# Kernel optimization log

Measured on AMD Instinct MI355X. Metric: run time of the kernel, lower is better.

## Reference

```python
import jax, jax.numpy as jnp
import numpy as np

WH, WW = 7, 7
NUM_HEADS = 16
DIM = 512
NW = 64  # windows per image (56/7)^2


def _relative_position_index(wh, ww):
    coords = np.stack(np.meshgrid(np.arange(wh), np.arange(ww), indexing='ij'))  # 2,wh,ww
    cf = coords.reshape(2, -1)
    rel = cf[:, :, None] - cf[:, None, :]            # 2,N,N
    rel = rel.transpose(1, 2, 0).astype(np.int32)    # N,N,2
    rel[:, :, 0] += wh - 1
    rel[:, :, 1] += ww - 1
    rel[:, :, 0] *= 2 * ww - 1
    return jnp.asarray(rel.sum(-1))                  # N,N int32


def setup_inputs() -> dict:
    key = jax.random.key(0)
    ks = jax.random.split(key, 7)
    B_, N, C = 2048, WH * WW, DIM
    x = jax.random.normal(ks[0], (B_, N, C), dtype=jnp.float32)
    # 0 / -100 shifted-window mask pattern
    mask = jnp.where(jax.random.uniform(ks[1], (NW, N, N)) < 0.8, 0.0, -100.0).astype(jnp.float32)
    qkv_w = jax.random.normal(ks[2], (3 * C, C), dtype=jnp.float32) * 0.02
    qkv_b = jax.random.normal(ks[3], (3 * C,), dtype=jnp.float32) * 0.02
    proj_w = jax.random.normal(ks[4], (C, C), dtype=jnp.float32) * 0.02
    proj_b = jax.random.normal(ks[5], (C,), dtype=jnp.float32) * 0.02
    rel_bias_table = jax.random.normal(ks[6], ((2 * WH - 1) * (2 * WW - 1), NUM_HEADS), dtype=jnp.float32) * 0.02
    rel_index = _relative_position_index(WH, WW)
    return {"x": x, "mask": mask, "qkv_w": qkv_w, "qkv_b": qkv_b,
            "proj_w": proj_w, "proj_b": proj_b,
            "rel_bias_table": rel_bias_table, "rel_index": rel_index}


def reference(x, mask, qkv_w, qkv_b, proj_w, proj_b, rel_bias_table, rel_index):
    B_, N, C = x.shape
    H = NUM_HEADS
    hd = C // H
    scale = hd ** -0.5
    qkv = x @ qkv_w.T + qkv_b                         # B_,N,3C
    qkv = qkv.reshape(B_, N, 3, H, hd).transpose(2, 0, 3, 1, 4)  # 3,B_,H,N,hd
    q, k, v = qkv[0] * scale, qkv[1], qkv[2]
    attn = jnp.einsum('bhnd,bhmd->bhnm', q, k)        # B_,H,N,N
    # gathered relative position bias -> H,N,N
    bias = rel_bias_table[rel_index.reshape(-1)].reshape(N, N, H).transpose(2, 0, 1)
    attn = attn + bias[None]
    nW = mask.shape[0]
    attn = attn.reshape(B_ // nW, nW, H, N, N) + mask[None, :, None]
    attn = jax.nn.softmax(attn.reshape(B_, H, N, N), axis=-1)
    out = jnp.einsum('bhnm,bhmd->bhnd', attn, v).transpose(0, 2, 1, 3).reshape(B_, N, C)
    return out @ proj_w.T + proj_b
```

## Files before the change

kernel.cpp:

```cpp
#include <hip/hip_runtime.h>

typedef unsigned short u16;
typedef short s16x8 __attribute__((ext_vector_type(8)));
typedef __bf16 bf16x8 __attribute__((ext_vector_type(8)));
typedef float f32x4 __attribute__((ext_vector_type(4)));


__device__ __forceinline__ u16 f2bf(float f) {
  union { float f; unsigned u; } x; x.f = f;
  unsigned r = (x.u + 0x7fffu + ((x.u >> 16) & 1u)) >> 16;
  return (u16)r;
}

__device__ __forceinline__ f32x4 mfma_bf16_16x16x32(s16x8 a, s16x8 b, f32x4 c) {
  return __builtin_amdgcn_mfma_f32_16x16x32_bf16(
      __builtin_bit_cast(bf16x8, a), __builtin_bit_cast(bf16x8, b), c, 0, 0, 0);
}

__device__ __forceinline__ void gl_lds16(const u16* g, u16* l) {
  __builtin_amdgcn_global_load_lds(
      (__attribute__((address_space(1))) unsigned int*)g,
      (__attribute__((address_space(3))) unsigned int*)l, 16, 0, 0);
}


__global__ __launch_bounds__(256) void cvt_bf16(const float* __restrict__ src,
                                                u16* __restrict__ dst, int n) {
  int i = (blockIdx.x * 256 + threadIdx.x) * 4;
  if (i + 3 < n) {
    float4 f = *(const float4*)(src + i);
    ushort4 o;
    o.x = f2bf(f.x); o.y = f2bf(f.y); o.z = f2bf(f.z); o.w = f2bf(f.w);
    *(ushort4*)(dst + i) = o;
  }
}

__global__ __launch_bounds__(256) void build_bias(const float* __restrict__ tbl,
                                                  const int* __restrict__ ridx,
                                                  float* __restrict__ biasf) {
  int t = blockIdx.x * 256 + threadIdx.x;
  if (t < 16 * 2401) {
    int h = t / 2401, ij = t % 2401;
    biasf[t] = tbl[ridx[ij] * 16 + h];
  }
}


template <bool OUT_BF16>
__global__ __launch_bounds__(256) void gemm_bt(const u16* __restrict__ A,
                                               const u16* __restrict__ B,
                                               const float* __restrict__ bias,
                                               void* __restrict__ C,
                                               int M, int N, int K) {
  __shared__ u16 As[128 * 32];
  __shared__ u16 Bs[128 * 32];
  const int t = threadIdx.x;
  const int w = t >> 6, l = t & 63;
  const int quad = l >> 4, lo = l & 15;
  const long m0 = (long)blockIdx.y * 128;
  const long n0 = (long)blockIdx.x * 128;
  const int wm = (w >> 1) * 64, wn = (w & 1) * 64;

  f32x4 acc[4][4] = {};

  const int srow0 = w * 32 + (l >> 2);
  const int skc = (l & 3) * 8;
  const u16* gA = A + (m0 + srow0) * (long)K + skc;
  const u16* gB = B + (n0 + srow0) * (long)K + skc;
  u16* lA = As + (w * 128 + l) * 8;
  u16* lB = Bs + (w * 128 + l) * 8;

  for (int k0 = 0; k0 < K; k0 += 32) {
    gl_lds16(gA + k0, lA);
    gl_lds16(gA + 16 * (long)K + k0, lA + 64 * 8);
    gl_lds16(gB + k0, lB);
    gl_lds16(gB + 16 * (long)K + k0, lB + 64 * 8);
    __syncthreads();

    s16x8 af[4], bfv[4];
#pragma unroll
    for (int i = 0; i < 4; ++i) {
      af[i]  = *(const s16x8*)(As + (wm + i * 16 + lo) * 32 + quad * 8);
      bfv[i] = *(const s16x8*)(Bs + (wn + i * 16 + lo) * 32 + quad * 8);
    }
#pragma unroll
    for (int mt = 0; mt < 4; ++mt)
#pragma unroll
      for (int nt = 0; nt < 4; ++nt)
        acc[mt][nt] = mfma_bf16_16x16x32(af[mt], bfv[nt], acc[mt][nt]);
    __syncthreads();
  }

#pragma unroll
  for (int mt = 0; mt < 4; ++mt) {
#pragma unroll
    for (int nt = 0; nt < 4; ++nt) {
      long col = n0 + wn + nt * 16 + lo;
      float bv = bias[col];
      long rowb = m0 + wm + mt * 16 + quad * 4;
#pragma unroll
      for (int r = 0; r < 4; ++r) {
        float v = acc[mt][nt][r] + bv;
        long off = (rowb + r) * (long)N + col;
        if (OUT_BF16) ((u16*)C)[off] = f2bf(v);
        else          ((float*)C)[off] = v;
      }
    }
  }
}


__global__ __launch_bounds__(256) void attn_kernel(const u16* __restrict__ qkv,
                                                   const float* __restrict__ biasf,
                                                   const float* __restrict__ mask,
                                                   u16* __restrict__ ao) {
  __shared__ u16 P[4][64 * 64];
  const int t = threadIdx.x;
  const int w = t >> 6, l = t & 63;
  const int quad = l >> 4, lo = l & 15;
  const int u = blockIdx.x * 4 + w;
  const int b = u >> 4, h = u & 15;

  const u16* qp = qkv + (long)b * 49 * 1536 + h * 32;
  const u16* kp = qp + 512;
  const u16* vp = qp + 1024;

  const s16x8 zero8 = {};
  s16x8 qf[4], kf[4];
#pragma unroll
  for (int mt = 0; mt < 4; ++mt) {
    int m = mt * 16 + lo;
    qf[mt] = (m < 49) ? *(const s16x8*)(qp + (long)m * 1536 + quad * 8) : zero8;
    kf[mt] = (m < 49) ? *(const s16x8*)(kp + (long)m * 1536 + quad * 8) : zero8;
  }

  f32x4 S[4][4] = {};
#pragma unroll
  for (int mt = 0; mt < 4; ++mt)
#pragma unroll
    for (int nt = 0; nt < 4; ++nt)
      S[mt][nt] = mfma_bf16_16x16x32(qf[mt], kf[nt], S[mt][nt]);

  const float scale = 0.17677669529663687f;
  const float* bh = biasf + h * 2401;
  const float* mw = mask + (long)(b & 63) * 2401;

#pragma unroll
  for (int mt = 0; mt < 4; ++mt) {
#pragma unroll
    for (int r = 0; r < 4; ++r) {
      int row = mt * 16 + quad * 4 + r;
      int rr = row < 49 ? row : 48;
      float vals[4];
#pragma unroll
      for (int nt = 0; nt < 4; ++nt) {
        int col = nt * 16 + lo;
        vals[nt] = (col < 49)
                       ? S[mt][nt][r] * scale + bh[rr * 49 + col] + mw[rr * 49 + col]
                       : -1e30f;
      }
      float rm = fmaxf(fmaxf(vals[0], vals[1]), fmaxf(vals[2], vals[3]));
#pragma unroll
      for (int off = 1; off < 16; off <<= 1) rm = fmaxf(rm, __shfl_xor(rm, off, 16));
      float s = 0.f;
#pragma unroll
      for (int nt = 0; nt < 4; ++nt) {
        vals[nt] = __expf(vals[nt] - rm);
        s += vals[nt];
      }
#pragma unroll
      for (int off = 1; off < 16; off <<= 1) s += __shfl_xor(s, off, 16);
      float is = 1.f / s;
#pragma unroll
      for (int nt = 0; nt < 4; ++nt) S[mt][nt][r] = vals[nt] * is;
    }
  }

  u16* pw = &P[w][0];
#pragma unroll
  for (int mt = 0; mt < 4; ++mt)
#pragma unroll
    for (int nt = 0; nt < 4; ++nt)
#pragma unroll
      for (int r = 0; r < 4; ++r)
        pw[(mt * 16 + quad * 4 + r) * 64 + nt * 16 + lo] = f2bf(S[mt][nt][r]);

  f32x4 O[4][2] = {};
#pragma unroll
  for (int kt = 0; kt < 2; ++kt) {
    s16x8 vb[2];
#pragma unroll
    for (int nt = 0; nt < 2; ++nt) {
      union { u16 us[8]; s16x8 v; } tb;
#pragma unroll
      for (int jj = 0; jj < 8; ++jj) {
        int j = kt * 32 + quad * 8 + jj;
        tb.us[jj] = (j < 49) ? vp[(long)j * 1536 + nt * 16 + lo] : (u16)0;
      }
      vb[nt] = tb.v;
    }
#pragma unroll
    for (int mt = 0; mt < 4; ++mt) {
      s16x8 pa = *(const s16x8*)(pw + (mt * 16 + lo) * 64 + kt * 32 + quad * 8);
      O[mt][0] = mfma_bf16_16x16x32(pa, vb[0], O[mt][0]);
      O[mt][1] = mfma_bf16_16x16x32(pa, vb[1], O[mt][1]);
    }
  }

  u16* op = ao + (long)b * 49 * 512 + h * 32;
#pragma unroll
  for (int mt = 0; mt < 4; ++mt)
#pragma unroll
    for (int nt = 0; nt < 2; ++nt)
#pragma unroll
      for (int r = 0; r < 4; ++r) {
        int row = mt * 16 + quad * 4 + r;
        if (row < 49) op[(long)row * 512 + nt * 16 + lo] = f2bf(O[mt][nt][r]);
      }
}


extern "C" void kernel_launch(void* const* d_in, const int* in_sizes, int n_in,
                              void* d_out, int out_size, void* d_ws, size_t ws_size,
                              hipStream_t stream) {
  const float* x      = (const float*)d_in[0];
  const float* mask   = (const float*)d_in[1];
  const float* qkv_w  = (const float*)d_in[2];
  const float* qkv_b  = (const float*)d_in[3];
  const float* proj_w = (const float*)d_in[4];
  const float* proj_b = (const float*)d_in[5];
  const float* tbl    = (const float*)d_in[6];
  const int*   ridx   = (const int*)d_in[7];

  u16* xb    = (u16*)d_ws;
  u16* qkvb  = xb + 51380224;
  u16* wq    = qkvb + 154140672;
  u16* wp    = wq + 786432;
  float* biasf = (float*)(wp + 262144);

  cvt_bf16<<<50176, 256, 0, stream>>>(x, xb, 51380224);
  cvt_bf16<<<768, 256, 0, stream>>>(qkv_w, wq, 786432);
  cvt_bf16<<<256, 256, 0, stream>>>(proj_w, wp, 262144);
  build_bias<<<151, 256, 0, stream>>>(tbl, ridx, biasf);

  gemm_bt<true><<<dim3(12, 784), 256, 0, stream>>>(xb, wq, qkv_b, qkvb,
                                                   100352, 1536, 512);
  attn_kernel<<<8192, 256, 0, stream>>>(qkvb, biasf, mask, xb);

  gemm_bt<false><<<dim3(4, 784), 256, 0, stream>>>(xb, wp, proj_b, d_out,
                                                   100352, 512, 512);
}
```

Baseline: 933.8 us.

## Swizzle LDS layouts, remap GEMM block order, and vectorize epilogue stores

XOR-swizzles the LDS tiles in the GEMM and the P tile in attention to cut bank conflicts on the fragment reads. It remaps the GEMM workgroup order for better L2 locality. It also swaps the MFMA operand order so each lane holds four consecutive output columns, which lets the GEMM and attention epilogues write 8- or 16-byte vectors instead of scattered scalar stores. This adds some index arithmetic, and the changed output layout must stay consistent across the GEMMs and the attention kernel.

```diff
diff --git a/kernel.cpp b/kernel.cpp
--- a/kernel.cpp
+++ b/kernel.cpp
@@ -21,6 +21,10 @@
   __builtin_amdgcn_global_load_lds(
       (__attribute__((address_space(1))) unsigned int*)g,
       (__attribute__((address_space(3))) unsigned int*)l, 16, 0, 0);
+}
+
+__device__ __forceinline__ int p_idx(int row, int col) {
+  return row * 64 + ((((col >> 3) ^ (row & 7)) << 3) | (col & 7));
 }
 
 
@@ -57,14 +61,25 @@
   const int t = threadIdx.x;
   const int w = t >> 6, l = t & 63;
   const int quad = l >> 4, lo = l & 15;
-  const long m0 = (long)blockIdx.y * 128;
-  const long n0 = (long)blockIdx.x * 128;
+
+  int bx = blockIdx.x, by = blockIdx.y;
+  {
+    const int nwg = gridDim.x * gridDim.y;
+    if ((nwg & 7) == 0) {
+      const int lin = bx + gridDim.x * by;
+      const int swz = (lin & 7) * (nwg >> 3) + (lin >> 3);
+      bx = swz % gridDim.x;
+      by = swz / gridDim.x;
+    }
+  }
+  const long m0 = (long)by * 128;
+  const long n0 = (long)bx * 128;
   const int wm = (w >> 1) * 64, wn = (w & 1) * 64;
 
   f32x4 acc[4][4] = {};
 
   const int srow0 = w * 32 + (l >> 2);
-  const int skc = (l & 3) * 8;
+  const int skc = ((l & 3) ^ ((srow0 >> 1) & 3)) * 8;
   const u16* gA = A + (m0 + srow0) * (long)K + skc;
   const u16* gB = B + (n0 + srow0) * (long)K + skc;
   u16* lA = As + (w * 128 + l) * 8;
@@ -80,30 +95,39 @@
     s16x8 af[4], bfv[4];
 #pragma unroll
     for (int i = 0; i < 4; ++i) {
-      af[i]  = *(const s16x8*)(As + (wm + i * 16 + lo) * 32 + quad * 8);
-      bfv[i] = *(const s16x8*)(Bs + (wn + i * 16 + lo) * 32 + quad * 8);
+      const int ra = wm + i * 16 + lo;
+      const int rb = wn + i * 16 + lo;
+      af[i]  = *(const s16x8*)(As + ra * 32 + ((quad ^ ((ra >> 1) & 3)) << 3));
+      bfv[i] = *(const s16x8*)(Bs + rb * 32 + ((quad ^ ((rb >> 1) & 3)) << 3));
     }
 #pragma unroll
     for (int mt = 0; mt < 4; ++mt)
 #pragma unroll
       for (int nt = 0; nt < 4; ++nt)
-        acc[mt][nt] = mfma_bf16_16x16x32(af[mt], bfv[nt], acc[mt][nt]);
+        acc[mt][nt] = mfma_bf16_16x16x32(bfv[nt], af[mt], acc[mt][nt]);
     __syncthreads();
   }
 
 #pragma unroll
   for (int mt = 0; mt < 4; ++mt) {
+    const long m = m0 + wm + mt * 16 + lo;
 #pragma unroll
     for (int nt = 0; nt < 4; ++nt) {
-      long col = n0 + wn + nt * 16 + lo;
-      float bv = bias[col];
-      long rowb = m0 + wm + mt * 16 + quad * 4;
-#pragma unroll
-      for (int r = 0; r < 4; ++r) {
-        float v = acc[mt][nt][r] + bv;
-        long off = (rowb + r) * (long)N + col;
-        if (OUT_BF16) ((u16*)C)[off] = f2bf(v);
-        else          ((float*)C)[off] = v;
+      const long n = n0 + wn + nt * 16 + quad * 4;
+      const float4 bv = *(const float4*)(bias + n);
+      const float v0 = acc[mt][nt][0] + bv.x;
+      const float v1 = acc[mt][nt][1] + bv.y;
+      const float v2 = acc[mt][nt][2] + bv.z;
+      const float v3 = acc[mt][nt][3] + bv.w;
+      const long off = m * (long)N + n;
+      if (OUT_BF16) {
+        uint2 o;
+        o.x = (unsigned)f2bf(v0) | ((unsigned)f2bf(v1) << 16);
+        o.y = (unsigned)f2bf(v2) | ((unsigned)f2bf(v3) << 16);
+        *(uint2*)((u16*)C + off) = o;
+      } else {
+        float4 o = make_float4(v0, v1, v2, v3);
+        *(float4*)((float*)C + off) = o;
       }
     }
   }
@@ -183,7 +207,7 @@
     for (int nt = 0; nt < 4; ++nt)
 #pragma unroll
       for (int r = 0; r < 4; ++r)
-        pw[(mt * 16 + quad * 4 + r) * 64 + nt * 16 + lo] = f2bf(S[mt][nt][r]);
+        pw[p_idx(mt * 16 + quad * 4 + r, nt * 16 + lo)] = f2bf(S[mt][nt][r]);
 
   f32x4 O[4][2] = {};
 #pragma unroll
@@ -201,22 +225,27 @@
     }
 #pragma unroll
     for (int mt = 0; mt < 4; ++mt) {
-      s16x8 pa = *(const s16x8*)(pw + (mt * 16 + lo) * 64 + kt * 32 + quad * 8);
-      O[mt][0] = mfma_bf16_16x16x32(pa, vb[0], O[mt][0]);
-      O[mt][1] = mfma_bf16_16x16x32(pa, vb[1], O[mt][1]);
+      s16x8 pa = *(const s16x8*)(pw + p_idx(mt * 16 + lo, kt * 32 + quad * 8));
+      O[mt][0] = mfma_bf16_16x16x32(vb[0], pa, O[mt][0]);
+      O[mt][1] = mfma_bf16_16x16x32(vb[1], pa, O[mt][1]);
     }
   }
 
   u16* op = ao + (long)b * 49 * 512 + h * 32;
 #pragma unroll
-  for (int mt = 0; mt < 4; ++mt)
-#pragma unroll
-    for (int nt = 0; nt < 2; ++nt)
-#pragma unroll
-      for (int r = 0; r < 4; ++r) {
-        int row = mt * 16 + quad * 4 + r;
-        if (row < 49) op[(long)row * 512 + nt * 16 + lo] = f2bf(O[mt][nt][r]);
-      }
+  for (int mt = 0; mt < 4; ++mt) {
+    const int q = mt * 16 + lo;
+    if (q < 49) {
+#pragma unroll
+      for (int nt = 0; nt < 2; ++nt) {
+        const int d = nt * 16 + quad * 4;
+        uint2 o;
+        o.x = (unsigned)f2bf(O[mt][nt][0]) | ((unsigned)f2bf(O[mt][nt][1]) << 16);
+        o.y = (unsigned)f2bf(O[mt][nt][2]) | ((unsigned)f2bf(O[mt][nt][3]) << 16);
+        *(uint2*)(op + (long)q * 512 + d) = o;
+      }
+    }
+  }
 }
 
 
```

Measured after the change: 1.031 ms. 1.1x slower.

## Double-buffer GEMM LDS tiles, swizzle LDS layouts, and remap workgroups for locality

Applied to the files above, without the earlier changes.

The GEMM now double-buffers its A/B LDS tiles, prefetching the next K-slice while the MFMAs run on the current one, and keeps only one barrier per iteration. It XOR-swizzles the LDS chunk placement to cut bank conflicts on fragment reads. It also remaps the workgroup index so that consecutive blocks spread across tiles, aimed at better L2/MALL locality. The attention kernel's P buffer gets an XOR-swizzled layout to cut bank conflicts. In exchange, GEMM LDS use doubles, which may lower occupancy.

```diff
diff --git a/kernel.cpp b/kernel.cpp
--- a/kernel.cpp
+++ b/kernel.cpp
@@ -21,6 +21,10 @@
   __builtin_amdgcn_global_load_lds(
       (__attribute__((address_space(1))) unsigned int*)g,
       (__attribute__((address_space(3))) unsigned int*)l, 16, 0, 0);
+}
+
+__device__ __forceinline__ int p_idx(int row, int col) {
+  return row * 64 + ((((col >> 3) ^ (row & 7)) << 3) | (col & 7));
 }
 
 
@@ -52,43 +56,70 @@
                                                const float* __restrict__ bias,
                                                void* __restrict__ C,
                                                int M, int N, int K) {
-  __shared__ u16 As[128 * 32];
-  __shared__ u16 Bs[128 * 32];
+  __shared__ u16 As[2][128 * 32];
+  __shared__ u16 Bs[2][128 * 32];
   const int t = threadIdx.x;
   const int w = t >> 6, l = t & 63;
   const int quad = l >> 4, lo = l & 15;
-  const long m0 = (long)blockIdx.y * 128;
-  const long n0 = (long)blockIdx.x * 128;
+
+  int bx = blockIdx.x, by = blockIdx.y;
+  {
+    const int nwg = gridDim.x * gridDim.y;
+    if ((nwg & 7) == 0) {
+      const int lin = bx + gridDim.x * by;
+      const int swz = (lin & 7) * (nwg >> 3) + (lin >> 3);
+      bx = swz % gridDim.x;
+      by = swz / gridDim.x;
+    }
+  }
+  const long m0 = (long)by * 128;
+  const long n0 = (long)bx * 128;
   const int wm = (w >> 1) * 64, wn = (w & 1) * 64;
 
   f32x4 acc[4][4] = {};
 
   const int srow0 = w * 32 + (l >> 2);
-  const int skc = (l & 3) * 8;
+  const int skc = ((l & 3) ^ ((srow0 >> 1) & 3)) * 8;
   const u16* gA = A + (m0 + srow0) * (long)K + skc;
   const u16* gB = B + (n0 + srow0) * (long)K + skc;
-  u16* lA = As + (w * 128 + l) * 8;
-  u16* lB = Bs + (w * 128 + l) * 8;
-
-  for (int k0 = 0; k0 < K; k0 += 32) {
-    gl_lds16(gA + k0, lA);
-    gl_lds16(gA + 16 * (long)K + k0, lA + 64 * 8);
-    gl_lds16(gB + k0, lB);
-    gl_lds16(gB + 16 * (long)K + k0, lB + 64 * 8);
-    __syncthreads();
-
+  const int lofs = (w * 128 + l) * 8;
+
+  const int NT = K >> 5;
+
+  gl_lds16(gA, As[0] + lofs);
+  gl_lds16(gA + 16 * (long)K, As[0] + lofs + 64 * 8);
+  gl_lds16(gB, Bs[0] + lofs);
+  gl_lds16(gB + 16 * (long)K, Bs[0] + lofs + 64 * 8);
+  __syncthreads();
+
+  int cur = 0;
+  for (int t0 = 0; t0 < NT; ++t0) {
+    if (t0 + 1 < NT) {
+      const int k0 = (t0 + 1) << 5;
+      gl_lds16(gA + k0, As[cur ^ 1] + lofs);
+      gl_lds16(gA + 16 * (long)K + k0, As[cur ^ 1] + lofs + 64 * 8);
+      gl_lds16(gB + k0, Bs[cur ^ 1] + lofs);
+      gl_lds16(gB + 16 * (long)K + k0, Bs[cur ^ 1] + lofs + 64 * 8);
+    }
+
+    const u16* as = As[cur];
+    const u16* bs = Bs[cur];
     s16x8 af[4], bfv[4];
 #pragma unroll
     for (int i = 0; i < 4; ++i) {
-      af[i]  = *(const s16x8*)(As + (wm + i * 16 + lo) * 32 + quad * 8);
-      bfv[i] = *(const s16x8*)(Bs + (wn + i * 16 + lo) * 32 + quad * 8);
+      const int ra = wm + i * 16 + lo;
+      const int rb = wn + i * 16 + lo;
+      af[i]  = *(const s16x8*)(as + ra * 32 + ((quad ^ ((ra >> 1) & 3)) << 3));
+      bfv[i] = *(const s16x8*)(bs + rb * 32 + ((quad ^ ((rb >> 1) & 3)) << 3));
     }
 #pragma unroll
     for (int mt = 0; mt < 4; ++mt)
 #pragma unroll
       for (int nt = 0; nt < 4; ++nt)
         acc[mt][nt] = mfma_bf16_16x16x32(af[mt], bfv[nt], acc[mt][nt]);
+
     __syncthreads();
+    cur ^= 1;
   }
 
 #pragma unroll
@@ -183,7 +214,7 @@
     for (int nt = 0; nt < 4; ++nt)
 #pragma unroll
       for (int r = 0; r < 4; ++r)
-        pw[(mt * 16 + quad * 4 + r) * 64 + nt * 16 + lo] = f2bf(S[mt][nt][r]);
+        pw[p_idx(mt * 16 + quad * 4 + r, nt * 16 + lo)] = f2bf(S[mt][nt][r]);
 
   f32x4 O[4][2] = {};
 #pragma unroll
@@ -201,7 +232,7 @@
     }
 #pragma unroll
     for (int mt = 0; mt < 4; ++mt) {
-      s16x8 pa = *(const s16x8*)(pw + (mt * 16 + lo) * 64 + kt * 32 + quad * 8);
+      s16x8 pa = *(const s16x8*)(pw + p_idx(mt * 16 + lo, kt * 32 + quad * 8));
       O[mt][0] = mfma_bf16_16x16x32(pa, vb[0], O[mt][0]);
       O[mt][1] = mfma_bf16_16x16x32(pa, vb[1], O[mt][1]);
     }
```

New measurement: 899.5 us. -3.7%, faster.
